# Optimization experiments

Measured on AMD Instinct MI355X. Metric: run time of the kernel, lower is better.

## Reference

```python
import jax, jax.numpy as jnp
import numpy as np

# ---- dims ----
N = 100000      # nodes
E = 1000000     # directed edges
F_IN = 64       # num_features
H = 64          # nhid
G = 256         # graphs in batch
C = 8           # num_classes
K = 3           # propagation hops
ALPHA = 0.5     # residual coefficient passed to conv1 in the torch forward


def setup_inputs() -> dict:
    key = jax.random.key(0)
    ks = jax.random.split(key, 16)
    x = jax.random.normal(ks[0], (N, F_IN), dtype=jnp.float32)
    edge_index = jax.random.randint(ks[1], (2, E), 0, N, dtype=jnp.int32)
    batch = jnp.sort(jax.random.randint(ks[2], (N,), 0, G, dtype=jnp.int32))

    def lin(k, fi, fo):
        bound = 1.0 / np.sqrt(fi)
        kw, kb = jax.random.split(k)
        W = jax.random.uniform(kw, (fi, fo), jnp.float32, -bound, bound)
        b = jax.random.uniform(kb, (fo,), jnp.float32, -bound, bound)
        return W, b

    W_sgc, b_sgc = lin(ks[3], F_IN, H)   # SGC linear
    w_att, b_att = lin(ks[4], H, 1)      # readout attention gate
    W1, b1 = lin(ks[5], 2 * H, H)
    W2, b2 = lin(ks[6], H, H // 2)
    W3, b3 = lin(ks[7], H // 2, C)
    return {"x": x, "edge_index": edge_index, "batch": batch,
            "W_sgc": W_sgc, "b_sgc": b_sgc, "w_att": w_att, "b_att": b_att,
            "W1": W1, "b1": b1, "W2": W2, "b2": b2, "W3": W3, "b3": b3}


def reference(x, edge_index, batch, W_sgc, b_sgc, w_att, b_att,
              W1, b1, W2, b2, W3, b3):
    n = x.shape[0]
    # GCN-normalized adjacency with self-loops (standard SGC propagation)
    loops = jnp.arange(n, dtype=edge_index.dtype)
    row = jnp.concatenate([edge_index[0], loops])
    col = jnp.concatenate([edge_index[1], loops])
    deg = jax.ops.segment_sum(jnp.ones_like(row, dtype=x.dtype), row, num_segments=n)
    dinv = jax.lax.rsqrt(jnp.maximum(deg, 1.0))
    norm = dinv[row] * dinv[col]                     # [E+N]

    # SGC_DAT2: linear transform, then K hops with alpha residual (APPNP-style)
    h0 = x @ W_sgc + b_sgc                           # [N, H]
    h = h0
    for _ in range(K):
        agg = jax.ops.segment_sum(norm[:, None] * h[col], row, num_segments=n)
        h = (1.0 - ALPHA) * agg + ALPHA * h0
    h = jax.nn.relu(h)                               # dropout: eval mode, no-op

    # new_readout3: segment-softmax gated sum pool + global max pool
    v = jax.nn.sigmoid(h @ w_att + b_att)            # [N, 1]
    vmax = jax.ops.segment_max(v, batch, num_segments=G)
    ve = jnp.exp(v - vmax[batch])
    vsum = jax.ops.segment_sum(ve, batch, num_segments=G)
    v = ve / (vsum[batch] + 1e-16)
    gmp = jax.ops.segment_max(h, batch, num_segments=G)       # [G, H]
    gsp = jax.ops.segment_sum(v * h, batch, num_segments=G)   # [G, H]
    z = jnp.concatenate([gmp, gsp], axis=1)                   # [G, 2H]

    # MLP head (dropout no-op in eval)
    z = jax.nn.relu(z @ W1 + b1)
    z = jax.nn.relu(z @ W2 + b2)
    return jax.nn.log_softmax(z @ W3 + b3, axis=-1)           # [G, C]
```

## Files before the change

### kernel.cpp

```cpp
#include <hip/hip_runtime.h>
#include <math.h>

#define N_NODES 100000
#define N_EDGES 1000000
#define NGRAPH 256

#define NBUCK 196
#define BUCKN 512
#define BUCKCAP 8192
#define EPB 2048
#define NBIN_BLOCKS ((N_EDGES + EPB - 1) / EPB)
#define NBOUND_BLOCKS ((N_NODES + 255) / 256)
#define WINCAP 10240
#define DUMMY ((unsigned)N_NODES)
#define H0_BLOCKS ((N_NODES / 16 + 3) / 4)

typedef unsigned short ushort_t;
typedef __attribute__((ext_vector_type(2))) float floatx2;

__device__ __forceinline__ ushort_t f2bf(float f) {
    unsigned u = __float_as_uint(f);
    u += 0x7fffu + ((u >> 16) & 1u);
    return (ushort_t)(u >> 16);
}
__device__ __forceinline__ float bf2f(ushort_t u) {
    return __uint_as_float(((unsigned)u) << 16);
}
__device__ __forceinline__ float bf_lo(unsigned u) {
    return __uint_as_float(u << 16);
}
__device__ __forceinline__ float bf_hi(unsigned u) {
    return __uint_as_float(u & 0xffff0000u);
}
__device__ __forceinline__ unsigned pack2(float hi, float lo) {
    return ((unsigned)f2bf(hi) << 16) | (unsigned)f2bf(lo);
}
__device__ __forceinline__ floatx2 fp8x2_lo(unsigned u) {
    return __builtin_amdgcn_cvt_pk_f32_fp8(u, false);
}
__device__ __forceinline__ floatx2 fp8x2_hi(unsigned u) {
    return __builtin_amdgcn_cvt_pk_f32_fp8(u, true);
}
__device__ __forceinline__ ushort_t f32_fp8x2(float a, float b) {
    return (ushort_t)(__builtin_amdgcn_cvt_pk_fp8_f32(a, b, 0u, false) & 0xffffu);
}

using frag_ab = __attribute__((ext_vector_type(8))) short;
using frag_cd = __attribute__((ext_vector_type(4))) float;

__global__ __launch_bounds__(256) void k_bin_bounds_h0(const int* __restrict__ row,
        const int* __restrict__ col, int* __restrict__ gcursor,
        unsigned* __restrict__ slab,
        const int* __restrict__ batch, int* __restrict__ gbound,
        const float* __restrict__ x, const float* __restrict__ W,
        const float* __restrict__ bias, ushort_t* __restrict__ h0b) {
    __shared__ int lcount[NBUCK];
    __shared__ int lbase[NBUCK];
    __shared__ int sexcl[NBUCK];
    __shared__ int sc[256];
    __shared__ unsigned staged[EPB];
    __shared__ int sdelta[EPB];
    int t = threadIdx.x;
    int b = blockIdx.x;
    if (b >= NBIN_BLOCKS + NBOUND_BLOCKS) {
        int wid = ((b - NBIN_BLOCKS - NBOUND_BLOCKS) * 256 + t) >> 6;
        if (wid >= N_NODES / 16) return;
        int lane = t & 63;
        int row0 = wid * 16;
        int m = lane & 15, q = lane >> 4;

        frag_ab bfr[2][4];
#pragma unroll
        for (int ks = 0; ks < 2; ++ks)
#pragma unroll
            for (int nt = 0; nt < 4; ++nt)
#pragma unroll
                for (int j = 0; j < 8; ++j)
                    bfr[ks][nt][j] = (short)f2bf(W[(ks * 32 + q * 8 + j) * 64 + nt * 16 + m]);

        frag_ab afr[2];
#pragma unroll
        for (int ks = 0; ks < 2; ++ks) {
            const float4* xp = (const float4*)(x + (size_t)(row0 + m) * 64 + ks * 32 + q * 8);
            float4 v0 = xp[0], v1 = xp[1];
            afr[ks][0] = (short)f2bf(v0.x); afr[ks][1] = (short)f2bf(v0.y);
            afr[ks][2] = (short)f2bf(v0.z); afr[ks][3] = (short)f2bf(v0.w);
            afr[ks][4] = (short)f2bf(v1.x); afr[ks][5] = (short)f2bf(v1.y);
            afr[ks][6] = (short)f2bf(v1.z); afr[ks][7] = (short)f2bf(v1.w);
        }

        frag_cd acc[4];
#pragma unroll
        for (int nt = 0; nt < 4; ++nt) acc[nt] = (frag_cd){0.f, 0.f, 0.f, 0.f};
#pragma unroll
        for (int ks = 0; ks < 2; ++ks)
#pragma unroll
            for (int nt = 0; nt < 4; ++nt)
                acc[nt] = __builtin_amdgcn_mfma_f32_16x16x32_bf16(afr[ks], bfr[ks][nt], acc[nt], 0, 0, 0);

#pragma unroll
        for (int nt = 0; nt < 4; ++nt) {
            int cc = nt * 16 + m;
            float bl = bias[cc];
#pragma unroll
            for (int r = 0; r < 4; ++r) {
                int rr = row0 + q * 4 + r;
                h0b[(size_t)rr * 64 + cc] = f2bf(acc[nt][r] + bl);
            }
        }
        return;
    }
    if (b >= NBIN_BLOCKS) {
        int n = (b - NBIN_BLOCKS) * 256 + t;
        if (n >= N_NODES) return;
        int bb = batch[n];
        int prev = (n == 0) ? -1 : batch[n - 1];
        for (int g = prev + 1; g <= bb; ++g) gbound[g] = n;
        if (n == N_NODES - 1) {
            for (int g = bb + 1; g <= NGRAPH; ++g) gbound[g] = N_NODES;
        }
        return;
    }
    for (int i = t; i < NBUCK; i += 256) lcount[i] = 0;
    __syncthreads();
    int base = b * EPB;
    unsigned rec[8]; int bp[8];
#pragma unroll
    for (int k = 0; k < 8; ++k) {
        int e = base + k * 256 + t;
        if (e < N_EDGES) {
            int r = row[e], c = col[e];
            int bk = r >> 9;
            int pos = atomicAdd(&lcount[bk], 1);
            rec[k] = ((unsigned)(r & 511) << 17) | (unsigned)c;
            bp[k] = (bk << 16) | pos;
        } else bp[k] = -1;
    }
    __syncthreads();
    int v = (t < NBUCK) ? lcount[t] : 0;
    if (t < NBUCK) lbase[t] = (v > 0) ? atomicAdd(&gcursor[t], v) : 0;
    sc[t] = v; __syncthreads();
    for (int off = 1; off < 256; off <<= 1) {
        int u = (t >= off) ? sc[t - off] : 0;
        __syncthreads();
        sc[t] += u;
        __syncthreads();
    }
    int excl = sc[t] - v;
    if (t < NBUCK) {
        sexcl[t] = excl;
        lbase[t] = t * BUCKCAP + lbase[t] - excl;
    }
    __syncthreads();
#pragma unroll
    for (int k = 0; k < 8; ++k) {
        if (bp[k] >= 0) {
            int bk = bp[k] >> 16, pos = bp[k] & 0xffff;
            int slot = sexcl[bk] + pos;
            staged[slot] = rec[k];
            sdelta[slot] = lbase[bk];
        }
    }
    __syncthreads();
    int total = sc[255];
    for (int i = t; i < total; i += 256)
        slab[sdelta[i] + i] = staged[i];
}

__global__ __launch_bounds__(256) void k_build_scale(const unsigned* __restrict__ slab,
        const int* __restrict__ gcursor,
        int* __restrict__ start, int* __restrict__ counts, float* __restrict__ dinv,
        unsigned* __restrict__ csr4,
        const ushort_t* __restrict__ h0b, unsigned char* __restrict__ h0s) {
    __shared__ int ncount[BUCKN];
    __shared__ int nstart[BUCKN];
    __shared__ int sc[256];
    __shared__ float sdv[BUCKN];
    int b = blockIdx.x, t = threadIdx.x;
    int cnt = gcursor[b];
    int ebase = b * WINCAP;
    int node0 = b * BUCKN;
    int nn = min(BUCKN, N_NODES - node0);
    for (int i = t; i < nn; i += 256) ncount[i] = 0;
    __syncthreads();
    const unsigned* sl = slab + (size_t)b * BUCKCAP;
    for (int i = t; i < cnt; i += 256)
        atomicAdd(&ncount[sl[i] >> 17], 1);
    __syncthreads();
    int c0 = (2 * t < nn) ? ncount[2 * t] : 0;
    int c1 = (2 * t + 1 < nn) ? ncount[2 * t + 1] : 0;
    int p0 = (c0 + 15) & ~15, p1 = (c1 + 15) & ~15;
    int ps = p0 + p1;
    sc[t] = ps; __syncthreads();
    for (int off = 1; off < 256; off <<= 1) {
        int v = (t >= off) ? sc[t - off] : 0;
        __syncthreads();
        sc[t] += v;
        __syncthreads();
    }
    int ex = sc[t] - ps;
    if (2 * t < nn) nstart[2 * t] = ex;
    if (2 * t + 1 < nn) nstart[2 * t + 1] = ex + p0;
    __syncthreads();
    for (int i = t; i < nn; i += 256) {
        int node = node0 + i;
        int c = ncount[i];
        int pc = (c + 15) & ~15;
        int st = ebase + nstart[i];
        start[node] = st;
        counts[node] = pc;
        float dv = rsqrtf((float)(c + 1));
        dinv[node] = dv;
        sdv[i] = dv;
        for (int k = c; k < pc; ++k) csr4[st + k] = DUMMY;
    }
    __syncthreads();
    for (int i = t; i < cnt; i += 256) {
        unsigned r = sl[i];
        int pos = atomicAdd(&nstart[r >> 17], 1);
        csr4[ebase + pos] = r & 0x1ffffu;
    }
    const uint4* hp = (const uint4*)h0b;
    uint2* op = (uint2*)h0s;
    int nch = nn * 8;
    for (int i = t; i < nch; i += 256) {
        float dv = sdv[i >> 3];
        uint4 vch = hp[(size_t)node0 * 8 + i];
        ushort_t s0 = f32_fp8x2(bf_lo(vch.x) * dv, bf_hi(vch.x) * dv);
        ushort_t s1 = f32_fp8x2(bf_lo(vch.y) * dv, bf_hi(vch.y) * dv);
        ushort_t s2 = f32_fp8x2(bf_lo(vch.z) * dv, bf_hi(vch.z) * dv);
        ushort_t s3 = f32_fp8x2(bf_lo(vch.w) * dv, bf_hi(vch.w) * dv);
        uint2 o;
        o.x = (unsigned)s0 | ((unsigned)s1 << 16);
        o.y = (unsigned)s2 | ((unsigned)s3 << 16);
        op[(size_t)node0 * 8 + i] = o;
    }
    if (b == 0 && t < 16) ((unsigned*)(h0s + (size_t)N_NODES * 64))[t] = 0;
}

__device__ __forceinline__ void hop_sum4(int node, int l,
        const unsigned* __restrict__ hs_in, const int* __restrict__ start,
        const int* __restrict__ counts, const unsigned* __restrict__ csr4,
        float& a0, float& a1, float& a2, float& a3) {
    unsigned su = hs_in[node * 16 + l];
    floatx2 slo = fp8x2_lo(su), shi = fp8x2_hi(su);
    a0 = slo.x; a1 = slo.y; a2 = shi.x; a3 = shi.y;
    int st = start[node], cnt = counts[node];
    for (int j = 0; j < cnt; j += 16) {
        const uint4* cp = (const uint4*)(csr4 + st + j);
        uint4 g0 = cp[0];
        uint4 g1 = cp[1];
        uint4 g2 = cp[2];
        uint4 g3 = cp[3];
        unsigned w0  = hs_in[g0.x * 16 + l];
        unsigned w1  = hs_in[g0.y * 16 + l];
        unsigned w2  = hs_in[g0.z * 16 + l];
        unsigned w3  = hs_in[g0.w * 16 + l];
        unsigned w4  = hs_in[g1.x * 16 + l];
        unsigned w5  = hs_in[g1.y * 16 + l];
        unsigned w6  = hs_in[g1.z * 16 + l];
        unsigned w7  = hs_in[g1.w * 16 + l];
        unsigned w8  = hs_in[g2.x * 16 + l];
        unsigned w9  = hs_in[g2.y * 16 + l];
        unsigned w10 = hs_in[g2.z * 16 + l];
        unsigned w11 = hs_in[g2.w * 16 + l];
        unsigned w12 = hs_in[g3.x * 16 + l];
        unsigned w13 = hs_in[g3.y * 16 + l];
        unsigned w14 = hs_in[g3.z * 16 + l];
        unsigned w15 = hs_in[g3.w * 16 + l];
        float s0 = 0.f, s1 = 0.f, s2 = 0.f, s3 = 0.f;
        unsigned wv[16] = {w0, w1, w2, w3, w4, w5, w6, w7,
                           w8, w9, w10, w11, w12, w13, w14, w15};
#pragma unroll
        for (int k = 0; k < 16; ++k) {
            floatx2 lo = fp8x2_lo(wv[k]), hi = fp8x2_hi(wv[k]);
            s0 += lo.x; s1 += lo.y; s2 += hi.x; s3 += hi.y;
        }
        a0 += s0; a1 += s1; a2 += s2; a3 += s3;
    }
}

__global__ void k_hop(const unsigned* __restrict__ hs_in, const unsigned* __restrict__ hs0,
                      const float* __restrict__ dinv, const int* __restrict__ start,
                      const int* __restrict__ counts, const unsigned* __restrict__ csr4,
                      unsigned* __restrict__ hs_out) {
    int node = blockIdx.x * 16 + ((int)threadIdx.x >> 4);
    int l = threadIdx.x & 15;
    float a0, a1, a2, a3;
    hop_sum4(node, l, hs_in, start, counts, csr4, a0, a1, a2, a3);
    float di = dinv[node];
    float c = 0.5f * di * di;
    unsigned ru = hs0[node * 16 + l];
    floatx2 rlo = fp8x2_lo(ru), rhi = fp8x2_hi(ru);
    ushort_t lo = f32_fp8x2(c * a0 + 0.5f * rlo.x, c * a1 + 0.5f * rlo.y);
    ushort_t hi = f32_fp8x2(c * a2 + 0.5f * rhi.x, c * a3 + 0.5f * rhi.y);
    hs_out[node * 16 + l] = (unsigned)lo | ((unsigned)hi << 16);
    if (blockIdx.x == 0 && threadIdx.x < 16)
        hs_out[N_NODES * 16 + threadIdx.x] = 0;
}

__global__ void k_hop_final(const unsigned* __restrict__ hs_in, const uint2* __restrict__ h0b2,
                            const float* __restrict__ dinv, const int* __restrict__ start,
                            const int* __restrict__ counts, const unsigned* __restrict__ csr4,
                            const float* __restrict__ w_att, const float* __restrict__ b_att,
                            uint2* __restrict__ h_out2, float* __restrict__ v_raw) {
    int node = blockIdx.x * 16 + ((int)threadIdx.x >> 4);
    int l = threadIdx.x & 15;
    float a0, a1, a2, a3;
    hop_sum4(node, l, hs_in, start, counts, csr4, a0, a1, a2, a3);
    float cdi = 0.5f * dinv[node];
    uint2 u = h0b2[node * 16 + l];
    float h0v = fmaxf(cdi * a0 + 0.5f * bf_lo(u.x), 0.f);
    float h1v = fmaxf(cdi * a1 + 0.5f * bf_hi(u.x), 0.f);
    float h2v = fmaxf(cdi * a2 + 0.5f * bf_lo(u.y), 0.f);
    float h3v = fmaxf(cdi * a3 + 0.5f * bf_hi(u.y), 0.f);
    uint2 o; o.x = pack2(h1v, h0v); o.y = pack2(h3v, h2v);
    h_out2[node * 16 + l] = o;
    float4 wa = *(const float4*)(w_att + 4 * l);
    float pp = (h0v * wa.x + h1v * wa.y) + (h2v * wa.z + h3v * wa.w);
#pragma unroll
    for (int off = 8; off >= 1; off >>= 1) pp += __shfl_xor(pp, off, 64);
    if (l == 0) {
        v_raw[node] = 1.f / (1.f + expf(-(pp + b_att[0])));
    }
}

__global__ void k_readout_mlp(const ushort_t* __restrict__ hb, const float* __restrict__ v_raw,
        const int* __restrict__ gbound,
        const float* __restrict__ W1, const float* __restrict__ b1,
        const float* __restrict__ W2, const float* __restrict__ b2,
        const float* __restrict__ W3, const float* __restrict__ b3,
        float* __restrict__ out) {
    int g = blockIdx.x, t = threadIdx.x;
    int s = gbound[g], e = gbound[g + 1];
    __shared__ float red[256];

    float m = -3.402823466e38f;
    for (int n = s + t; n < e; n += 256) m = fmaxf(m, v_raw[n]);
    red[t] = m; __syncthreads();
    for (int off = 128; off >= 1; off >>= 1) {
        if (t < off) red[t] = fmaxf(red[t], red[t + off]);
        __syncthreads();
    }
    float vmax = red[0]; __syncthreads();

    float ss = 0.f;
    for (int n = s + t; n < e; n += 256) ss += expf(v_raw[n] - vmax);
    red[t] = ss; __syncthreads();
    for (int off = 128; off >= 1; off >>= 1) {
        if (t < off) red[t] += red[t + off];
        __syncthreads();
    }
    float inv = 1.f / (red[0] + 1e-16f);
    __syncthreads();

    int wv = t >> 6, lane = t & 63;
    float gm = -3.402823466e38f, gs = 0.f;
    for (int n = s + wv; n < e; n += 4) {
        float hv = bf2f(hb[(size_t)n * 64 + lane]);
        float vn = expf(v_raw[n] - vmax) * inv;
        gm = fmaxf(gm, hv);
        gs += vn * hv;
    }
    __shared__ float pm[4][64], ps[4][64];
    pm[wv][lane] = gm; ps[wv][lane] = gs;
    __syncthreads();

    __shared__ float z[128];
    if (t < 64) {
        z[t] = fmaxf(fmaxf(pm[0][t], pm[1][t]), fmaxf(pm[2][t], pm[3][t]));
        z[64 + t] = ps[0][t] + ps[1][t] + ps[2][t] + ps[3][t];
    }
    __syncthreads();

    __shared__ float z1[64];
    if (t < 64) {
        float a = b1[t];
#pragma unroll 8
        for (int k = 0; k < 128; ++k) a += z[k] * W1[k * 64 + t];
        z1[t] = fmaxf(a, 0.f);
    }
    __syncthreads();
    __shared__ float z2[32];
    if (t < 32) {
        float a = b2[t];
#pragma unroll 8
        for (int k = 0; k < 64; ++k) a += z1[k] * W2[k * 32 + t];
        z2[t] = fmaxf(a, 0.f);
    }
    __syncthreads();
    __shared__ float z3[8];
    if (t < 8) {
        float a = b3[t];
#pragma unroll
        for (int k = 0; k < 32; ++k) a += z2[k] * W3[k * 8 + t];
        z3[t] = a;
    }
    __syncthreads();
    if (t == 0) {
        float mx = z3[0];
#pragma unroll
        for (int j = 1; j < 8; ++j) mx = fmaxf(mx, z3[j]);
        float se = 0.f;
#pragma unroll
        for (int j = 0; j < 8; ++j) se += expf(z3[j] - mx);
        float lse = mx + logf(se);
#pragma unroll
        for (int j = 0; j < 8; ++j) out[g * 8 + j] = z3[j] - lse;
    }
}

extern "C" void kernel_launch(void* const* d_in, const int* in_sizes, int n_in,
                              void* d_out, int out_size, void* d_ws, size_t ws_size,
                              hipStream_t stream) {
    const float* x     = (const float*)d_in[0];
    const int*   edge  = (const int*)d_in[1];
    const int*   row   = edge;
    const int*   col   = edge + N_EDGES;
    const int*   batch = (const int*)d_in[2];
    const float* W_sgc = (const float*)d_in[3];
    const float* b_sgc = (const float*)d_in[4];
    const float* w_att = (const float*)d_in[5];
    const float* b_att = (const float*)d_in[6];
    const float* W1    = (const float*)d_in[7];
    const float* b1    = (const float*)d_in[8];
    const float* W2    = (const float*)d_in[9];
    const float* b2    = (const float*)d_in[10];
    const float* W3    = (const float*)d_in[11];
    const float* b3    = (const float*)d_in[12];
    float* out = (float*)d_out;

    char* p = (char*)d_ws;
    auto alloc = [&](size_t bytes) {
        char* r = p;
        p += (bytes + 255) & ~(size_t)255;
        return r;
    };
    int*      gcursor = (int*)alloc((size_t)NBUCK * 4);
    int*      gbound  = (int*)alloc((size_t)(NGRAPH + 1) * 4);
    int*      start   = (int*)alloc((size_t)N_NODES * 4);
    int*      counts  = (int*)alloc((size_t)N_NODES * 4);
    float*    dinv    = (float*)alloc((size_t)N_NODES * 4);
    float*    vraw    = (float*)alloc((size_t)N_NODES * 4);
    ushort_t* h0b     = (ushort_t*)alloc((size_t)N_NODES * 64 * 2);
    unsigned char* h0s = (unsigned char*)alloc((size_t)(N_NODES + 1) * 64);
    ushort_t* hAs     = (ushort_t*)alloc((size_t)(N_NODES + 1) * 32 * 2);
    ushort_t* hBs     = (ushort_t*)alloc((size_t)(N_NODES + 1) * 32 * 2);
    ushort_t* hfin    = (ushort_t*)alloc((size_t)N_NODES * 64 * 2);
    unsigned* csr4    = (unsigned*)alloc(((size_t)NBUCK * WINCAP + 64) * 4);
    unsigned* slab    = (unsigned*)alloc((size_t)NBUCK * BUCKCAP * 4);

    hipMemsetAsync(gcursor, 0, (size_t)NBUCK * 4, stream);

    k_bin_bounds_h0<<<NBIN_BLOCKS + NBOUND_BLOCKS + H0_BLOCKS, 256, 0, stream>>>(
        row, col, gcursor, slab, batch, gbound, x, W_sgc, b_sgc, h0b);
    k_build_scale<<<NBUCK, 256, 0, stream>>>(slab, gcursor, start, counts, dinv, csr4,
                                             h0b, (unsigned char*)h0s);
    k_hop<<<N_NODES / 16, 256, 0, stream>>>((const unsigned*)h0s, (const unsigned*)h0s,
                                            dinv, start, counts, csr4, (unsigned*)hAs);
    k_hop<<<N_NODES / 16, 256, 0, stream>>>((const unsigned*)hAs, (const unsigned*)h0s,
                                            dinv, start, counts, csr4, (unsigned*)hBs);
    k_hop_final<<<N_NODES / 16, 256, 0, stream>>>((const unsigned*)hBs, (const uint2*)h0b,
                                                  dinv, start, counts, csr4,
                                                  w_att, b_att, (uint2*)hfin, vraw);
    k_readout_mlp<<<NGRAPH, 256, 0, stream>>>(hfin, vraw, gbound,
                                              W1, b1, W2, b2, W3, b3, out);
}
```

Measured before the change: 221.8 us.

## Fuse readout MLP into final hop via last-block-done counters; vectorize edge binning

The separate readout/MLP kernel is folded into the final hop kernel. Each block atomically adds its finished node count per graph to a gdone counter, and the block that completes a graph runs that graph's softmax pooling and MLP head. One kernel launch and its tail gap go away, at the cost of serialized tail work in whichever blocks finish graphs last and of relying on threadfence for visibility across blocks. The edge binning kernel now handles twice as many edges per block and reads them with int4 vector loads. The memset is widened so the new counters are zeroed along with gcursor.

```diff
diff --git a/kernel.cpp b/kernel.cpp
--- a/kernel.cpp
+++ b/kernel.cpp
@@ -8,7 +8,7 @@
 #define NBUCK 196
 #define BUCKN 512
 #define BUCKCAP 8192
-#define EPB 2048
+#define EPB 4096
 #define NBIN_BLOCKS ((N_EDGES + EPB - 1) / EPB)
 #define NBOUND_BLOCKS ((N_NODES + 255) / 256)
 #define WINCAP 10240
@@ -124,17 +124,35 @@
     for (int i = t; i < NBUCK; i += 256) lcount[i] = 0;
     __syncthreads();
     int base = b * EPB;
-    unsigned rec[8]; int bp[8];
-#pragma unroll
-    for (int k = 0; k < 8; ++k) {
-        int e = base + k * 256 + t;
-        if (e < N_EDGES) {
-            int r = row[e], c = col[e];
-            int bk = r >> 9;
-            int pos = atomicAdd(&lcount[bk], 1);
-            rec[k] = ((unsigned)(r & 511) << 17) | (unsigned)c;
-            bp[k] = (bk << 16) | pos;
-        } else bp[k] = -1;
+    unsigned rec[16]; int bp[16];
+#pragma unroll
+    for (int k = 0; k < 4; ++k) {
+        int e0 = base + k * 1024 + t * 4;
+        if (e0 + 4 <= N_EDGES) {
+            int4 r4 = *(const int4*)(row + e0);
+            int4 c4 = *(const int4*)(col + e0);
+            int rr[4] = {r4.x, r4.y, r4.z, r4.w};
+            int cc[4] = {c4.x, c4.y, c4.z, c4.w};
+#pragma unroll
+            for (int j = 0; j < 4; ++j) {
+                int bk = rr[j] >> 9;
+                int pos = atomicAdd(&lcount[bk], 1);
+                rec[k * 4 + j] = ((unsigned)(rr[j] & 511) << 17) | (unsigned)cc[j];
+                bp[k * 4 + j] = (bk << 16) | pos;
+            }
+        } else {
+#pragma unroll
+            for (int j = 0; j < 4; ++j) {
+                int e = e0 + j;
+                if (e < N_EDGES) {
+                    int r = row[e], c = col[e];
+                    int bk = r >> 9;
+                    int pos = atomicAdd(&lcount[bk], 1);
+                    rec[k * 4 + j] = ((unsigned)(r & 511) << 17) | (unsigned)c;
+                    bp[k * 4 + j] = (bk << 16) | pos;
+                } else bp[k * 4 + j] = -1;
+            }
+        }
     }
     __syncthreads();
     int v = (t < NBUCK) ? lcount[t] : 0;
@@ -153,7 +171,7 @@
     }
     __syncthreads();
 #pragma unroll
-    for (int k = 0; k < 8; ++k) {
+    for (int k = 0; k < 16; ++k) {
         if (bp[k] >= 0) {
             int bk = bp[k] >> 16, pos = bp[k] & 0xffff;
             int slot = sexcl[bk] + pos;
@@ -299,114 +317,141 @@
         hs_out[N_NODES * 16 + threadIdx.x] = 0;
 }
 
-__global__ void k_hop_final(const unsigned* __restrict__ hs_in, const uint2* __restrict__ h0b2,
-                            const float* __restrict__ dinv, const int* __restrict__ start,
-                            const int* __restrict__ counts, const unsigned* __restrict__ csr4,
-                            const float* __restrict__ w_att, const float* __restrict__ b_att,
-                            uint2* __restrict__ h_out2, float* __restrict__ v_raw) {
-    int node = blockIdx.x * 16 + ((int)threadIdx.x >> 4);
-    int l = threadIdx.x & 15;
-    float a0, a1, a2, a3;
-    hop_sum4(node, l, hs_in, start, counts, csr4, a0, a1, a2, a3);
-    float cdi = 0.5f * dinv[node];
-    uint2 u = h0b2[node * 16 + l];
-    float h0v = fmaxf(cdi * a0 + 0.5f * bf_lo(u.x), 0.f);
-    float h1v = fmaxf(cdi * a1 + 0.5f * bf_hi(u.x), 0.f);
-    float h2v = fmaxf(cdi * a2 + 0.5f * bf_lo(u.y), 0.f);
-    float h3v = fmaxf(cdi * a3 + 0.5f * bf_hi(u.y), 0.f);
-    uint2 o; o.x = pack2(h1v, h0v); o.y = pack2(h3v, h2v);
-    h_out2[node * 16 + l] = o;
-    float4 wa = *(const float4*)(w_att + 4 * l);
-    float pp = (h0v * wa.x + h1v * wa.y) + (h2v * wa.z + h3v * wa.w);
-#pragma unroll
-    for (int off = 8; off >= 1; off >>= 1) pp += __shfl_xor(pp, off, 64);
-    if (l == 0) {
-        v_raw[node] = 1.f / (1.f + expf(-(pp + b_att[0])));
-    }
-}
-
-__global__ void k_readout_mlp(const ushort_t* __restrict__ hb, const float* __restrict__ v_raw,
-        const int* __restrict__ gbound,
+__global__ __launch_bounds__(256, 4) void k_hop_final(const unsigned* __restrict__ hs_in,
+        const uint2* __restrict__ h0b2,
+        const float* __restrict__ dinv, const int* __restrict__ start,
+        const int* __restrict__ counts, const unsigned* __restrict__ csr4,
+        const float* __restrict__ w_att, const float* __restrict__ b_att,
+        uint2* __restrict__ h_out2, float* __restrict__ v_raw,
+        const int* __restrict__ batch, const int* __restrict__ gbound,
+        int* __restrict__ gdone,
         const float* __restrict__ W1, const float* __restrict__ b1,
         const float* __restrict__ W2, const float* __restrict__ b2,
         const float* __restrict__ W3, const float* __restrict__ b3,
         float* __restrict__ out) {
-    int g = blockIdx.x, t = threadIdx.x;
-    int s = gbound[g], e = gbound[g + 1];
+    int t = threadIdx.x;
+    int node0 = blockIdx.x * 16;
+    int node = node0 + (t >> 4);
+    int l = t & 15;
+    {
+        float a0, a1, a2, a3;
+        hop_sum4(node, l, hs_in, start, counts, csr4, a0, a1, a2, a3);
+        float cdi = 0.5f * dinv[node];
+        uint2 u = h0b2[node * 16 + l];
+        float h0v = fmaxf(cdi * a0 + 0.5f * bf_lo(u.x), 0.f);
+        float h1v = fmaxf(cdi * a1 + 0.5f * bf_hi(u.x), 0.f);
+        float h2v = fmaxf(cdi * a2 + 0.5f * bf_lo(u.y), 0.f);
+        float h3v = fmaxf(cdi * a3 + 0.5f * bf_hi(u.y), 0.f);
+        uint2 o; o.x = pack2(h1v, h0v); o.y = pack2(h3v, h2v);
+        h_out2[node * 16 + l] = o;
+        float4 wa = *(const float4*)(w_att + 4 * l);
+        float pp = (h0v * wa.x + h1v * wa.y) + (h2v * wa.z + h3v * wa.w);
+#pragma unroll
+        for (int off = 8; off >= 1; off >>= 1) pp += __shfl_xor(pp, off, 64);
+        if (l == 0) v_raw[node] = 1.f / (1.f + expf(-(pp + b_att[0])));
+    }
+    __syncthreads();
+
+    __shared__ int fin[20];
+    __shared__ int nfin;
+    if (t == 0) {
+        nfin = 0;
+        __threadfence();
+        int gl = batch[node0], gh = batch[node0 + 15];
+        for (int g = gl; g <= gh; ++g) {
+            int s = gbound[g], e = gbound[g + 1];
+            int c = min(e, node0 + 16) - max(s, node0);
+            if (c > 0) {
+                int old = atomicAdd(&gdone[g], c);
+                if (old + c == e - s) fin[nfin++] = g;
+            }
+        }
+        if (nfin > 0) __threadfence();
+    }
+    __syncthreads();
+    int nf = nfin;
+    if (nf == 0) return;
+
     __shared__ float red[256];
-
-    float m = -3.402823466e38f;
-    for (int n = s + t; n < e; n += 256) m = fmaxf(m, v_raw[n]);
-    red[t] = m; __syncthreads();
-    for (int off = 128; off >= 1; off >>= 1) {
-        if (t < off) red[t] = fmaxf(red[t], red[t + off]);
-        __syncthreads();
-    }
-    float vmax = red[0]; __syncthreads();
-
-    float ss = 0.f;
-    for (int n = s + t; n < e; n += 256) ss += expf(v_raw[n] - vmax);
-    red[t] = ss; __syncthreads();
-    for (int off = 128; off >= 1; off >>= 1) {
-        if (t < off) red[t] += red[t + off];
-        __syncthreads();
-    }
-    float inv = 1.f / (red[0] + 1e-16f);
-    __syncthreads();
-
-    int wv = t >> 6, lane = t & 63;
-    float gm = -3.402823466e38f, gs = 0.f;
-    for (int n = s + wv; n < e; n += 4) {
-        float hv = bf2f(hb[(size_t)n * 64 + lane]);
-        float vn = expf(v_raw[n] - vmax) * inv;
-        gm = fmaxf(gm, hv);
-        gs += vn * hv;
-    }
     __shared__ float pm[4][64], ps[4][64];
-    pm[wv][lane] = gm; ps[wv][lane] = gs;
-    __syncthreads();
-
     __shared__ float z[128];
-    if (t < 64) {
-        z[t] = fmaxf(fmaxf(pm[0][t], pm[1][t]), fmaxf(pm[2][t], pm[3][t]));
-        z[64 + t] = ps[0][t] + ps[1][t] + ps[2][t] + ps[3][t];
-    }
-    __syncthreads();
-
     __shared__ float z1[64];
-    if (t < 64) {
-        float a = b1[t];
+    __shared__ float z2[32];
+    __shared__ float z3[8];
+    const ushort_t* hb = (const ushort_t*)h_out2;
+    for (int fi = 0; fi < nf; ++fi) {
+        int g = fin[fi];
+        int s = gbound[g], e = gbound[g + 1];
+
+        float m = -3.402823466e38f;
+        for (int n = s + t; n < e; n += 256) m = fmaxf(m, v_raw[n]);
+        red[t] = m; __syncthreads();
+        for (int off = 128; off >= 1; off >>= 1) {
+            if (t < off) red[t] = fmaxf(red[t], red[t + off]);
+            __syncthreads();
+        }
+        float vmax = red[0]; __syncthreads();
+
+        float ss = 0.f;
+        for (int n = s + t; n < e; n += 256) ss += expf(v_raw[n] - vmax);
+        red[t] = ss; __syncthreads();
+        for (int off = 128; off >= 1; off >>= 1) {
+            if (t < off) red[t] += red[t + off];
+            __syncthreads();
+        }
+        float inv = 1.f / (red[0] + 1e-16f);
+        __syncthreads();
+
+        int wv = t >> 6, lane = t & 63;
+        float gm = -3.402823466e38f, gs = 0.f;
+        for (int n = s + wv; n < e; n += 4) {
+            float hv = bf2f(hb[(size_t)n * 64 + lane]);
+            float vn = expf(v_raw[n] - vmax) * inv;
+            gm = fmaxf(gm, hv);
+            gs += vn * hv;
+        }
+        pm[wv][lane] = gm; ps[wv][lane] = gs;
+        __syncthreads();
+
+        if (t < 64) {
+            z[t] = fmaxf(fmaxf(pm[0][t], pm[1][t]), fmaxf(pm[2][t], pm[3][t]));
+            z[64 + t] = ps[0][t] + ps[1][t] + ps[2][t] + ps[3][t];
+        }
+        __syncthreads();
+
+        if (t < 64) {
+            float a = b1[t];
 #pragma unroll 8
-        for (int k = 0; k < 128; ++k) a += z[k] * W1[k * 64 + t];
-        z1[t] = fmaxf(a, 0.f);
-    }
-    __syncthreads();
-    __shared__ float z2[32];
-    if (t < 32) {
-        float a = b2[t];
+            for (int k = 0; k < 128; ++k) a += z[k] * W1[k * 64 + t];
+            z1[t] = fmaxf(a, 0.f);
+        }
+        __syncthreads();
+        if (t < 32) {
+            float a = b2[t];
 #pragma unroll 8
-        for (int k = 0; k < 64; ++k) a += z1[k] * W2[k * 32 + t];
-        z2[t] = fmaxf(a, 0.f);
-    }
-    __syncthreads();
-    __shared__ float z3[8];
-    if (t < 8) {
-        float a = b3[t];
-#pragma unroll
-        for (int k = 0; k < 32; ++k) a += z2[k] * W3[k * 8 + t];
-        z3[t] = a;
-    }
-    __syncthreads();
-    if (t == 0) {
-        float mx = z3[0];
-#pragma unroll
-        for (int j = 1; j < 8; ++j) mx = fmaxf(mx, z3[j]);
-        float se = 0.f;
-#pragma unroll
-        for (int j = 0; j < 8; ++j) se += expf(z3[j] - mx);
-        float lse = mx + logf(se);
-#pragma unroll
-        for (int j = 0; j < 8; ++j) out[g * 8 + j] = z3[j] - lse;
+            for (int k = 0; k < 64; ++k) a += z1[k] * W2[k * 32 + t];
+            z2[t] = fmaxf(a, 0.f);
+        }
+        __syncthreads();
+        if (t < 8) {
+            float a = b3[t];
+#pragma unroll
+            for (int k = 0; k < 32; ++k) a += z2[k] * W3[k * 8 + t];
+            z3[t] = a;
+        }
+        __syncthreads();
+        if (t == 0) {
+            float mx = z3[0];
+#pragma unroll
+            for (int j = 1; j < 8; ++j) mx = fmaxf(mx, z3[j]);
+            float se = 0.f;
+#pragma unroll
+            for (int j = 0; j < 8; ++j) se += expf(z3[j] - mx);
+            float lse = mx + logf(se);
+#pragma unroll
+            for (int j = 0; j < 8; ++j) out[g * 8 + j] = z3[j] - lse;
+        }
+        __syncthreads();
     }
 }
 
@@ -437,6 +482,7 @@
         return r;
     };
     int*      gcursor = (int*)alloc((size_t)NBUCK * 4);
+    int*      gdone   = (int*)alloc((size_t)NGRAPH * 4);
     int*      gbound  = (int*)alloc((size_t)(NGRAPH + 1) * 4);
     int*      start   = (int*)alloc((size_t)N_NODES * 4);
     int*      counts  = (int*)alloc((size_t)N_NODES * 4);
@@ -450,7 +496,7 @@
     unsigned* csr4    = (unsigned*)alloc(((size_t)NBUCK * WINCAP + 64) * 4);
     unsigned* slab    = (unsigned*)alloc((size_t)NBUCK * BUCKCAP * 4);
 
-    hipMemsetAsync(gcursor, 0, (size_t)NBUCK * 4, stream);
+    hipMemsetAsync(gcursor, 0, (size_t)2048, stream);
 
     k_bin_bounds_h0<<<NBIN_BLOCKS + NBOUND_BLOCKS + H0_BLOCKS, 256, 0, stream>>>(
         row, col, gcursor, slab, batch, gbound, x, W_sgc, b_sgc, h0b);
@@ -462,7 +508,7 @@
                                             dinv, start, counts, csr4, (unsigned*)hBs);
     k_hop_final<<<N_NODES / 16, 256, 0, stream>>>((const unsigned*)hBs, (const uint2*)h0b,
                                                   dinv, start, counts, csr4,
-                                                  w_att, b_att, (uint2*)hfin, vraw);
-    k_readout_mlp<<<NGRAPH, 256, 0, stream>>>(hfin, vraw, gbound,
-                                              W1, b1, W2, b2, W3, b3, out);
-}
+                                                  w_att, b_att, (uint2*)hfin, vraw,
+                                                  batch, gbound, gdone,
+                                                  W1, b1, W2, b2, W3, b3, out);
+}
```

Result: slower. 487.2 us (+119.7%).
